# Kernel optimization log

Hardware: AMD Instinct MI355X
Metric: run time of the kernel (lower is better)

## Reference

```python
import jax, jax.numpy as jnp
import numpy as np
from jax import lax

V, E, H, K = 50000, 128, 256, 9
B, T = 64, 512


def setup_inputs() -> dict:
    key = jax.random.key(0)
    ks = jax.random.split(key, 16)
    s = 0.05
    return {
        "x": jax.random.randint(ks[0], (B, T), 0, V),
        "tags": jax.random.randint(ks[1], (B, T), 0, K),
        "mask": jnp.ones((B, T), dtype=bool),
        "embed_table": jax.random.normal(ks[2], (V, E), jnp.float32) * s,
        "w_ih_f": jax.random.normal(ks[3], (4 * H, E), jnp.float32) * s,
        "w_hh_f": jax.random.normal(ks[4], (4 * H, H), jnp.float32) * s,
        "b_ih_f": jax.random.normal(ks[5], (4 * H,), jnp.float32) * s,
        "b_hh_f": jax.random.normal(ks[6], (4 * H,), jnp.float32) * s,
        "w_ih_b": jax.random.normal(ks[7], (4 * H, E), jnp.float32) * s,
        "w_hh_b": jax.random.normal(ks[8], (4 * H, H), jnp.float32) * s,
        "b_ih_b": jax.random.normal(ks[9], (4 * H,), jnp.float32) * s,
        "b_hh_b": jax.random.normal(ks[10], (4 * H,), jnp.float32) * s,
        "w_tag": jax.random.normal(ks[11], (K, 2 * H), jnp.float32) * s,
        "b_tag": jax.random.normal(ks[12], (K,), jnp.float32) * s,
        "start_trans": jax.random.normal(ks[13], (K,), jnp.float32) * s,
        "end_trans": jax.random.normal(ks[14], (K,), jnp.float32) * s,
        "trans": jax.random.normal(ks[15], (K, K), jnp.float32) * s,
    }


def _lstm_dir(x_tbe, w_ih, w_hh, b_ih, b_hh, reverse=False):
    # x_tbe: [T, B, E]; torch gate order: i, f, g, o
    h0 = jnp.zeros((x_tbe.shape[1], H), x_tbe.dtype)
    c0 = jnp.zeros_like(h0)
    xg = jnp.einsum('tbe,ge->tbg', x_tbe, w_ih) + b_ih + b_hh  # precompute input gates

    def step(carry, xg_t):
        h, c = carry
        g = xg_t + h @ w_hh.T
        i, f, gg, o = jnp.split(g, 4, axis=-1)
        c = jax.nn.sigmoid(f) * c + jax.nn.sigmoid(i) * jnp.tanh(gg)
        h = jax.nn.sigmoid(o) * jnp.tanh(c)
        return (h, c), h

    _, hs = lax.scan(step, (h0, c0), xg, reverse=reverse)
    return hs  # [T, B, H]


def _crf_nll(emissions, tags, mask, start_trans, end_trans, trans):
    # emissions: [B,T,K]; tags: [B,T] int; mask: [B,T] bool. torchcrf, reduction='sum'.
    Bc, Tc, Kc = emissions.shape
    maskf = mask.astype(emissions.dtype)
    barange = jnp.arange(Bc)
    # numerator: score of gold path
    em_scores = jnp.take_along_axis(emissions, tags[..., None], axis=-1)[..., 0]  # [B,T]
    trans_scores = trans[tags[:, :-1], tags[:, 1:]]  # [B,T-1]
    num = start_trans[tags[:, 0]] + em_scores[:, 0]
    num = num + jnp.sum((em_scores[:, 1:] + trans_scores) * maskf[:, 1:], axis=1)
    last_idx = (jnp.sum(maskf, axis=1) - 1).astype(jnp.int32)
    last_tags = tags[barange, last_idx]
    num = num + end_trans[last_tags]
    # denominator: forward algorithm (log partition)
    alpha0 = start_trans[None, :] + emissions[:, 0]  # [B,K]

    def step(alpha, inp):
        em_t, m_t = inp  # [B,K], [B]
        nxt = jax.nn.logsumexp(alpha[:, :, None] + trans[None] + em_t[:, None, :], axis=1)
        return jnp.where(m_t[:, None], nxt, alpha), None

    alpha, _ = lax.scan(step, alpha0,
                        (jnp.swapaxes(emissions[:, 1:], 0, 1), mask[:, 1:].T))
    denom = jax.nn.logsumexp(alpha + end_trans[None, :], axis=1)
    llh = jnp.sum(num - denom)  # reduction='sum'
    return -llh


def reference(x, tags, mask, embed_table,
              w_ih_f, w_hh_f, b_ih_f, b_hh_f,
              w_ih_b, w_hh_b, b_ih_b, b_hh_b,
              w_tag, b_tag, start_trans, end_trans, trans):
    embedded = embed_table[x]                     # [B,T,E]
    x_tbe = jnp.swapaxes(embedded, 0, 1)          # [T,B,E]
    h_f = _lstm_dir(x_tbe, w_ih_f, w_hh_f, b_ih_f, b_hh_f, reverse=False)
    h_b = _lstm_dir(x_tbe, w_ih_b, w_hh_b, b_ih_b, b_hh_b, reverse=True)
    lstm_out = jnp.concatenate([h_f, h_b], axis=-1)         # [T,B,2H]
    lstm_out = jnp.swapaxes(lstm_out, 0, 1)                 # [B,T,2H]
    emissions = jnp.einsum('btd,kd->btk', lstm_out, w_tag) + b_tag
    return _crf_nll(emissions, tags, mask, start_trans, end_trans, trans)
```

## Files before the change

### kernel.cpp

```cpp
#include <hip/hip_runtime.h>
#include <stdint.h>


#define TT 512
#define BB 64
#define EE 128
#define HH 256

typedef __attribute__((ext_vector_type(8))) short short8;
typedef __attribute__((ext_vector_type(4))) float floatx4;
typedef __attribute__((ext_vector_type(2))) float floatx2;
typedef __attribute__((ext_vector_type(4))) unsigned uintx4;
typedef __attribute__((ext_vector_type(8))) unsigned uintx8;

__device__ __forceinline__ unsigned short f2bf(float f) {
    union { float f; unsigned u; } c; c.f = f;
    return (unsigned short)((c.u + 0x7FFFu + ((c.u >> 16) & 1u)) >> 16);
}
__device__ __forceinline__ unsigned pk_fp8x4(float a, float b, float c, float d) {
    int v = __builtin_amdgcn_cvt_pk_fp8_f32(a, b, 0, false);
    v = __builtin_amdgcn_cvt_pk_fp8_f32(c, d, v, true);
    return (unsigned)v;
}

__global__ __launch_bounds__(256)
void prep_kernel(const float* __restrict__ whf, const float* __restrict__ whb,
                 const float* __restrict__ wihf, const float* __restrict__ wihb,
                 unsigned* __restrict__ wre, unsigned short* __restrict__ wih_bf)
{
    const int bid = blockIdx.x, tid = threadIdx.x;
    if (bid < 512) {
        int idx = bid * 256 + tid;
        int j4   = idx & 7;
        int gcb  = (idx >> 3) & 7;
        int lane = (idx >> 6) & 63;
        int K0   = (idx >> 12) & 1;
        int wv   = (idx >> 13) & 7;
        int dir  = idx >> 16;
        int g = gcb >> 1, cb = gcb & 1;
        int l15 = lane & 15, lh = lane >> 4;
        int grow = g * 256 + wv * 32 + cb * 16 + l15;
        int k0 = K0 * 128 + lh * 32 + j4 * 4;
        const float* w = dir ? whb : whf;
        const float4 v = *(const float4*)(w + (size_t)grow * HH + k0);
        wre[idx] = pk_fp8x4(v.x, v.y, v.z, v.w);
    } else {
        int idx = (bid - 512) * 256 + tid;
        int dir = idx >> 14, rem = idx & 16383;
        const float* w = dir ? wihb : wihf;
        const float* s = w + (size_t)rem * 8;
        short8 v;
        #pragma unroll
        for (int j = 0; j < 8; ++j) v[j] = (short)f2bf(s[j]);
        *(short8*)(wih_bf + (size_t)idx * 8) = v;
    }
}

__global__ __launch_bounds__(256, 2)
void xg_kernel(const int* __restrict__ x, const float* __restrict__ embed,
               const unsigned short* __restrict__ wih_bf,
               const float* __restrict__ b_ih_f, const float* __restrict__ b_hh_f,
               const float* __restrict__ b_ih_b, const float* __restrict__ b_hh_b,
               unsigned* __restrict__ xg2)
{
    const int bid = blockIdx.x;
    const int dir = bid >> 10, t4 = (bid >> 3) & 127, nt = bid & 7;
    const int tid = threadIdx.x, lane = tid & 63, wv = tid >> 6;
    const int l15 = lane & 15, lh = lane >> 4;
    const float* b_ih = dir ? b_ih_b : b_ih_f;
    const float* b_hh = dir ? b_hh_b : b_hh_f;

    __shared__ int xid[64];
    __shared__ __align__(16) unsigned short As[64][136];
    __shared__ __align__(16) unsigned char Fs[64][144];
    __shared__ float bsh[128];

    if (tid < 128) bsh[tid] = b_ih[nt * 128 + tid] + b_hh[nt * 128 + tid];

    short8 wfr[8][4];
    const unsigned short* wbase = wih_bf + (size_t)dir * 131072;
    #pragma unroll
    for (int mt = 0; mt < 8; ++mt) {
        int grow = nt * 128 + mt * 16 + l15;
        #pragma unroll
        for (int kt = 0; kt < 4; ++kt)
            wfr[mt][kt] = *(const short8*)(wbase + (size_t)grow * EE + kt * 32 + lh * 8);
    }

    for (int tt = 0; tt < 4; ++tt) {
        const int t = t4 * 4 + tt;
        __syncthreads();
        if (tid < 64) xid[tid] = x[tid * TT + t];
        __syncthreads();
        for (int i = tid; i < 2048; i += 256) {
            int b = i >> 5, seg = i & 31;
            float4 v = *(const float4*)(embed + (size_t)xid[b] * EE + seg * 4);
            union { unsigned short u[4]; unsigned long long q; } p;
            p.u[0] = f2bf(v.x); p.u[1] = f2bf(v.y); p.u[2] = f2bf(v.z); p.u[3] = f2bf(v.w);
            *(unsigned long long*)&As[b][seg * 4] = p.q;
        }
        __syncthreads();

        floatx4 acc[8];
        #pragma unroll
        for (int mt = 0; mt < 8; ++mt) acc[mt] = (floatx4){0.f, 0.f, 0.f, 0.f};
        #pragma unroll
        for (int kt = 0; kt < 4; ++kt) {
            short8 af = *(const short8*)&As[wv * 16 + l15][kt * 32 + lh * 8];
            #pragma unroll
            for (int mt = 0; mt < 8; ++mt)
                acc[mt] = __builtin_amdgcn_mfma_f32_16x16x32_bf16(wfr[mt][kt], af, acc[mt], 0, 0, 0);
        }
        #pragma unroll
        for (int mt = 0; mt < 8; ++mt) {
            int j0 = mt * 16 + lh * 4;
            unsigned u = pk_fp8x4(acc[mt][0] + bsh[j0], acc[mt][1] + bsh[j0 + 1],
                                  acc[mt][2] + bsh[j0 + 2], acc[mt][3] + bsh[j0 + 3]);
            *(unsigned*)&Fs[wv * 16 + l15][j0] = u;
        }
        __syncthreads();
        for (int i = tid; i < 2048; i += 256) {
            int b = i >> 5, jq = i & 31;
            unsigned v = *(const unsigned*)&Fs[b][jq * 4];
            int growq = nt * 128 + jq * 4;
            int g = growq >> 8, hcol4 = (growq & 255) >> 2;
            size_t o32 = (((size_t)(dir * TT + t) * 64 + b) * 4 + g) * 64 + hcol4;
            xg2[o32] = v;
        }
    }
}

#define WWPAIR(A0, A1, V)                                                     \
    asm volatile("v_accvgpr_write_b32 a" #A0 ", %0\n\t"                       \
                 "v_accvgpr_write_b32 a" #A1 ", %1"                           \
                 :: "v"((unsigned)(V)), "v"((unsigned)((V) >> 32))            \
                 : "a" #A0, "a" #A1)

#define MFMA128(N0, N7, ACC, HF)                                              \
    asm volatile("v_mfma_f32_16x16x128_f8f6f4 %0, a[" #N0 ":" #N7 "], %1, %0" \
                 : "+v"(ACC) : "v"(HF))

__global__ void __launch_bounds__(512)
__attribute__((amdgpu_waves_per_eu(2, 2)))
rec_kernel(const unsigned char* __restrict__ wre, const unsigned* __restrict__ xg2,
           unsigned* __restrict__ hout)
{
    const int dir = blockIdx.x & 1;
    const int bg  = blockIdx.x >> 1;
    const int tid = threadIdx.x, lane = tid & 63, wv = tid >> 6;
    const int l15 = lane & 15, lh = lane >> 4;
    const int bbase = bg * 2;

    __shared__ __align__(16) unsigned char hbuf[2][16][272];
    __shared__ __align__(16) float gseg[4 * 2 * 268];
    for (int i = tid; i < 2176; i += 512) ((int*)hbuf)[i] = 0;

    const unsigned char* wb = wre + (size_t)dir * 262144 + wv * 32768 + lane * 256;
    {
        ulonglong2 q0, q1;
#define LOADSLOT(OFF)                                                         \
        q0 = *(const ulonglong2*)(wb + (OFF));                                \
        q1 = *(const ulonglong2*)(wb + (OFF) + 16);
        LOADSLOT(0)     WWPAIR(0,1,q0.x);   WWPAIR(2,3,q0.y);   WWPAIR(4,5,q1.x);   WWPAIR(6,7,q1.y);
        LOADSLOT(32)    WWPAIR(8,9,q0.x);   WWPAIR(10,11,q0.y); WWPAIR(12,13,q1.x); WWPAIR(14,15,q1.y);
        LOADSLOT(64)    WWPAIR(16,17,q0.x); WWPAIR(18,19,q0.y); WWPAIR(20,21,q1.x); WWPAIR(22,23,q1.y);
        LOADSLOT(96)    WWPAIR(24,25,q0.x); WWPAIR(26,27,q0.y); WWPAIR(28,29,q1.x); WWPAIR(30,31,q1.y);
        LOADSLOT(128)   WWPAIR(32,33,q0.x); WWPAIR(34,35,q0.y); WWPAIR(36,37,q1.x); WWPAIR(38,39,q1.y);
        LOADSLOT(160)   WWPAIR(40,41,q0.x); WWPAIR(42,43,q0.y); WWPAIR(44,45,q1.x); WWPAIR(46,47,q1.y);
        LOADSLOT(192)   WWPAIR(48,49,q0.x); WWPAIR(50,51,q0.y); WWPAIR(52,53,q1.x); WWPAIR(54,55,q1.y);
        LOADSLOT(224)   WWPAIR(56,57,q0.x); WWPAIR(58,59,q0.y); WWPAIR(60,61,q1.x); WWPAIR(62,63,q1.y);
        LOADSLOT(16384) WWPAIR(64,65,q0.x); WWPAIR(66,67,q0.y); WWPAIR(68,69,q1.x); WWPAIR(70,71,q1.y);
        LOADSLOT(16416) WWPAIR(72,73,q0.x); WWPAIR(74,75,q0.y); WWPAIR(76,77,q1.x); WWPAIR(78,79,q1.y);
        LOADSLOT(16448) WWPAIR(80,81,q0.x); WWPAIR(82,83,q0.y); WWPAIR(84,85,q1.x); WWPAIR(86,87,q1.y);
        LOADSLOT(16480) WWPAIR(88,89,q0.x); WWPAIR(90,91,q0.y); WWPAIR(92,93,q1.x); WWPAIR(94,95,q1.y);
        LOADSLOT(16512) WWPAIR(96,97,q0.x);   WWPAIR(98,99,q0.y);   WWPAIR(100,101,q1.x); WWPAIR(102,103,q1.y);
        LOADSLOT(16544) WWPAIR(104,105,q0.x); WWPAIR(106,107,q0.y); WWPAIR(108,109,q1.x); WWPAIR(110,111,q1.y);
        LOADSLOT(16576) WWPAIR(112,113,q0.x); WWPAIR(114,115,q0.y); WWPAIR(116,117,q1.x); WWPAIR(118,119,q1.y);
        LOADSLOT(16608) WWPAIR(120,121,q0.x); WWPAIR(122,123,q0.y); WWPAIR(124,125,q1.x); WWPAIR(126,127,q1.y);
#undef LOADSLOT
    }

    float c = 0.f;

    const int eb = tid >> 8;
    const int ec = tid & 255;

    const unsigned char* xrb = (const unsigned char*)xg2
        + (size_t)(dir * TT + (dir ? TT - 1 : 0)) * 65536
        + (bbase + eb) * 1024 + ec;
    const int xstep = dir ? -65536 : 65536;
    unsigned char* hdst = (unsigned char*)hout
        + ((size_t)(dir * TT + (dir ? TT - 1 : 0)) * BB + bbase + eb) * 256 + ec;
    const int hstep = dir ? -16384 : 16384;

    const unsigned char* hbr = &hbuf[0][0][0];
    unsigned char* hbw = (unsigned char*)&hbuf[1][0][0];

    __syncthreads();

    for (int t = 0; t < TT; ++t) {
        unsigned char xs0 = xrb[0], xs1 = xrb[256], xs2 = xrb[512], xs3 = xrb[768];

        floatx4 acc[4][2];
        #pragma unroll
        for (int g = 0; g < 4; ++g)
            #pragma unroll
            for (int cb = 0; cb < 2; ++cb)
                acc[g][cb] = (floatx4){0.f, 0.f, 0.f, 0.f};
        asm volatile("s_nop 1");

        {
            const unsigned char* hrow = hbr + l15 * 272 + lh * 32;
            uintx8 hf0, hf1;
            ((uintx4*)&hf0)[0] = *(const uintx4*)(hrow);
            ((uintx4*)&hf0)[1] = *(const uintx4*)(hrow + 16);
            ((uintx4*)&hf1)[0] = *(const uintx4*)(hrow + 128);
            ((uintx4*)&hf1)[1] = *(const uintx4*)(hrow + 144);
            MFMA128(0,7,      acc[0][0], hf0); MFMA128(16,23,    acc[1][0], hf0);
            MFMA128(32,39,    acc[2][0], hf0); MFMA128(48,55,    acc[3][0], hf0);
            MFMA128(64,71,    acc[0][0], hf1); MFMA128(80,87,    acc[1][0], hf1);
            MFMA128(96,103,   acc[2][0], hf1); MFMA128(112,119,  acc[3][0], hf1);
            MFMA128(8,15,     acc[0][1], hf0); MFMA128(24,31,    acc[1][1], hf0);
            MFMA128(40,47,    acc[2][1], hf0); MFMA128(56,63,    acc[3][1], hf0);
            MFMA128(72,79,    acc[0][1], hf1); MFMA128(88,95,    acc[1][1], hf1);
            MFMA128(104,111,  acc[2][1], hf1); MFMA128(120,127,  acc[3][1], hf1);
        }
        asm volatile("s_nop 7\n\ts_nop 7\n\ts_nop 7\n\ts_nop 3");

        if (l15 < 2) {
            #pragma unroll
            for (int g = 0; g < 4; ++g) {
                float* gw = &gseg[(g * 2 + l15) * 268 + wv * 32 + lh * 4];
                *(floatx4*)(gw)      = acc[g][0];
                *(floatx4*)(gw + 16) = acc[g][1];
            }
        }
        __syncthreads();

        float gv0 = gseg[(0 * 2 + eb) * 268 + ec];
        float gv1 = gseg[(1 * 2 + eb) * 268 + ec];
        float gv2 = gseg[(2 * 2 + eb) * 268 + ec];
        float gv3 = gseg[(3 * 2 + eb) * 268 + ec];
        floatx2 xi2 = __builtin_amdgcn_cvt_pk_f32_fp8((int)(unsigned)xs0, false);
        floatx2 xf2 = __builtin_amdgcn_cvt_pk_f32_fp8((int)(unsigned)xs1, false);
        floatx2 xg2v = __builtin_amdgcn_cvt_pk_f32_fp8((int)(unsigned)xs2, false);
        floatx2 xo2 = __builtin_amdgcn_cvt_pk_f32_fp8((int)(unsigned)xs3, false);
        float iv = gv0 + xi2[0];
        float fv = gv1 + xf2[0];
        float gv = gv2 + xg2v[0];
        float ov = gv3 + xo2[0];
        float A  = __expf(-iv);
        float C2 = __expf(-fv);
        float B  = __expf(-2.f * gv);
        float E  = __expf(-ov);
        float s1 = 1.f + A, s2 = 1.f + B, s3 = 1.f + C2, s4 = 1.f - B;
        float m1   = s1 * s2;
        float nsum = __builtin_fmaf(s4, s3, c * m1);
        float den  = s3 * m1;
        float cv   = nsum * __builtin_amdgcn_rcpf(den);
        c = cv;
        float F  = __expf(-2.f * cv);
        float s5 = 1.f + E, s6 = 1.f + F, s7 = 1.f - F;
        float hv = s7 * __builtin_amdgcn_rcpf(s5 * s6);
        unsigned char h8 = (unsigned char)
            ((unsigned)__builtin_amdgcn_cvt_pk_fp8_f32(hv, hv, 0, false) & 0xFFu);
        hbw[eb * 272 + ec] = h8;
        __syncthreads();

        *hdst = h8;
        hdst += hstep;
        xrb += xstep;
        { const unsigned char* tmp = hbr; hbr = hbw; hbw = (unsigned char*)tmp; }
    }
}

__global__ __launch_bounds__(256)
void em_kernel(const unsigned* __restrict__ hout, const float* __restrict__ w_tag,
               const float* __restrict__ b_tag, float* __restrict__ em)
{
    const int bid = blockIdx.x;
    const int b = bid >> 2, tq = bid & 3;
    const int tid = threadIdx.x, lane = tid & 63, wv = tid >> 6;
    const int dsel = lane >> 5, dloc = (lane & 31) * 8;

    float w72[9][8];
    #pragma unroll
    for (int k = 0; k < 9; ++k) {
        const float* src = w_tag + k * 512 + dsel * 256 + dloc;
        float4 a = *(const float4*)src;
        float4 b4 = *(const float4*)(src + 4);
        w72[k][0] = a.x;  w72[k][1] = a.y;  w72[k][2] = a.z;  w72[k][3] = a.w;
        w72[k][4] = b4.x; w72[k][5] = b4.y; w72[k][6] = b4.z; w72[k][7] = b4.w;
    }
    float btg = (lane < 9) ? b_tag[lane] : 0.f;

    for (int tt = wv; tt < 128; tt += 4) {
        int t = tq * 128 + tt;
        const unsigned* hp = hout + ((size_t)(dsel * TT + t) * BB + b) * 64 + (lane & 31) * 2;
        unsigned u0 = hp[0], u1 = hp[1];
        float hf[8];
        { floatx2 a = __builtin_amdgcn_cvt_pk_f32_fp8((int)u0, false);
          floatx2 b2 = __builtin_amdgcn_cvt_pk_f32_fp8((int)u0, true);
          hf[0]=a[0]; hf[1]=a[1]; hf[2]=b2[0]; hf[3]=b2[1]; }
        { floatx2 a = __builtin_amdgcn_cvt_pk_f32_fp8((int)u1, false);
          floatx2 b2 = __builtin_amdgcn_cvt_pk_f32_fp8((int)u1, true);
          hf[4]=a[0]; hf[5]=a[1]; hf[6]=b2[0]; hf[7]=b2[1]; }
        float p[9];
        #pragma unroll
        for (int k = 0; k < 9; ++k) {
            float s = 0.f;
            #pragma unroll
            for (int j = 0; j < 8; ++j) s += hf[j] * w72[k][j];
            p[k] = s;
        }
        float res = 0.f;
        #pragma unroll
        for (int k = 0; k < 9; ++k) {
            float s = p[k];
            s += __shfl_xor(s, 1);  s += __shfl_xor(s, 2);  s += __shfl_xor(s, 4);
            s += __shfl_xor(s, 8);  s += __shfl_xor(s, 16); s += __shfl_xor(s, 32);
            if (lane == k) res = s;
        }
        if (lane < 9) em[((size_t)b * TT + t) * 9 + lane] = res + btg;
    }
}

__global__ __launch_bounds__(256)
void scan_kernel(const float* __restrict__ em, const int* __restrict__ tags,
                 const float* __restrict__ st, const float* __restrict__ et,
                 const float* __restrict__ tr, float* __restrict__ out)
{
    const int b = blockIdx.x, tid = threadIdx.x;
    __shared__ float ems[4608];
    __shared__ float red[256];
    for (int i = tid; i < 4608; i += 256) ems[i] = em[(size_t)b * 4608 + i];
    __syncthreads();

    float nacc = 0.f;
    for (int t = tid; t < TT; t += 256) {
        int tg = tags[b * TT + t];
        float v = ems[t * 9 + tg];
        if (t > 0) v += tr[tags[b * TT + t - 1] * 9 + tg];
        nacc += v;
    }
    red[tid] = nacc;
    __syncthreads();
    for (int s = 128; s > 0; s >>= 1) {
        if (tid < s) red[tid] += red[tid + s];
        __syncthreads();
    }
    float num = red[0] + st[tags[b * TT]] + et[tags[b * TT + TT - 1]];

    if (tid < 64) {
        int kp = tid;
        int kpe = kp < 9 ? kp : 8;
        float trr[9];
        #pragma unroll
        for (int k = 0; k < 9; ++k) trr[k] = tr[k * 9 + kpe];
        float alpha = st[kpe] + ems[kpe];
        for (int t = 1; t < TT; ++t) {
            float av[9], m = -1e30f;
            #pragma unroll
            for (int k = 0; k < 9; ++k) { av[k] = __shfl(alpha, k) + trr[k]; m = fmaxf(m, av[k]); }
            float ssum = 0.f;
            #pragma unroll
            for (int k = 0; k < 9; ++k) ssum += __expf(av[k] - m);
            alpha = ems[t * 9 + kpe] + m + __logf(ssum);
        }
        float v = (kp < 9) ? (alpha + et[kpe]) : -1e30f;
        float m = v;
        m = fmaxf(m, __shfl_xor(m, 1));
        m = fmaxf(m, __shfl_xor(m, 2));
        m = fmaxf(m, __shfl_xor(m, 4));
        m = fmaxf(m, __shfl_xor(m, 8));
        float s = (kp < 9) ? __expf(v - m) : 0.f;
        s += __shfl_xor(s, 1);
        s += __shfl_xor(s, 2);
        s += __shfl_xor(s, 4);
        s += __shfl_xor(s, 8);
        if (kp == 0) atomicAdd(out, (m + __logf(s)) - num);
    }
}

extern "C" void kernel_launch(void* const* d_in, const int* in_sizes, int n_in,
                              void* d_out, int out_size, void* d_ws, size_t ws_size,
                              hipStream_t stream) {
    (void)in_sizes; (void)n_in; (void)out_size; (void)ws_size;
    const int* x        = (const int*)d_in[0];
    const int* tags     = (const int*)d_in[1];
    const float* embed  = (const float*)d_in[3];
    const float* w_ih_f = (const float*)d_in[4];
    const float* w_hh_f = (const float*)d_in[5];
    const float* b_ih_f = (const float*)d_in[6];
    const float* b_hh_f = (const float*)d_in[7];
    const float* w_ih_b = (const float*)d_in[8];
    const float* w_hh_b = (const float*)d_in[9];
    const float* b_ih_b = (const float*)d_in[10];
    const float* b_hh_b = (const float*)d_in[11];
    const float* w_tag  = (const float*)d_in[12];
    const float* b_tag  = (const float*)d_in[13];
    const float* st     = (const float*)d_in[14];
    const float* et     = (const float*)d_in[15];
    const float* tr     = (const float*)d_in[16];

    unsigned*       wre    = (unsigned*)d_ws;
    unsigned short* wih_bf = (unsigned short*)((char*)d_ws + 524288);
    unsigned*       xg2    = (unsigned*)((char*)d_ws + 1048576);
    unsigned*       hh     = (unsigned*)((char*)d_ws + 1048576 + 67108864);
    float*          em     = (float*)d_ws;

    hipMemsetAsync(d_out, 0, sizeof(float), stream);
    hipLaunchKernelGGL(prep_kernel, dim3(640), dim3(256), 0, stream,
                       w_hh_f, w_hh_b, w_ih_f, w_ih_b, wre, wih_bf);
    hipLaunchKernelGGL(xg_kernel, dim3(2048), dim3(256), 0, stream,
                       x, embed, wih_bf, b_ih_f, b_hh_f, b_ih_b, b_hh_b, xg2);
    hipLaunchKernelGGL(rec_kernel, dim3(64), dim3(512), 0, stream,
                       (const unsigned char*)wre, xg2, hh);
    hipLaunchKernelGGL(em_kernel, dim3(256), dim3(256), 0, stream,
                       hh, w_tag, b_tag, em);
    hipLaunchKernelGGL(scan_kernel, dim3(64), dim3(256), 0, stream,
                       em, tags, st, et, tr, (float*)d_out);
}
```

Before: 798.8 us.

## Split recurrent kernel to one batch row per block across 128 blocks

The recurrent LSTM kernel now handles one batch element per block instead of two, and the grid grows from 64 to 128 blocks. Each block still runs the full MFMA over 16 padded rows, but only the first 256 threads do the gate math and write h. The aim is to spread the serial time-step chain over twice as many CUs, halving the elementwise tail each step. In exchange the weight register loads and the MFMA work are duplicated per block, and half the threads sit idle during the elementwise phase.

Measured after the change: 767.6 us. 3.9% less time.

```diff
diff --git a/kernel.cpp b/kernel.cpp
--- a/kernel.cpp
+++ b/kernel.cpp
@@ -149,10 +149,9 @@
     const int bg  = blockIdx.x >> 1;
     const int tid = threadIdx.x, lane = tid & 63, wv = tid >> 6;
     const int l15 = lane & 15, lh = lane >> 4;
-    const int bbase = bg * 2;
 
     __shared__ __align__(16) unsigned char hbuf[2][16][272];
-    __shared__ __align__(16) float gseg[4 * 2 * 268];
+    __shared__ __align__(16) float gseg[4 * 268];
     for (int i = tid; i < 2176; i += 512) ((int*)hbuf)[i] = 0;
 
     const unsigned char* wb = wre + (size_t)dir * 262144 + wv * 32768 + lane * 256;
@@ -182,15 +181,15 @@
 
     float c = 0.f;
 
-    const int eb = tid >> 8;
     const int ec = tid & 255;
+    const bool edo = (tid < 256);
 
     const unsigned char* xrb = (const unsigned char*)xg2
         + (size_t)(dir * TT + (dir ? TT - 1 : 0)) * 65536
-        + (bbase + eb) * 1024 + ec;
+        + bg * 1024 + ec;
     const int xstep = dir ? -65536 : 65536;
     unsigned char* hdst = (unsigned char*)hout
-        + ((size_t)(dir * TT + (dir ? TT - 1 : 0)) * BB + bbase + eb) * 256 + ec;
+        + ((size_t)(dir * TT + (dir ? TT - 1 : 0)) * BB + bg) * 256 + ec;
     const int hstep = dir ? -16384 : 16384;
 
     const unsigned char* hbr = &hbuf[0][0][0];
@@ -227,47 +226,50 @@
         }
         asm volatile("s_nop 7\n\ts_nop 7\n\ts_nop 7\n\ts_nop 3");
 
-        if (l15 < 2) {
+        if (l15 == 0) {
             #pragma unroll
             for (int g = 0; g < 4; ++g) {
-                float* gw = &gseg[(g * 2 + l15) * 268 + wv * 32 + lh * 4];
+                float* gw = &gseg[g * 268 + wv * 32 + lh * 4];
                 *(floatx4*)(gw)      = acc[g][0];
                 *(floatx4*)(gw + 16) = acc[g][1];
             }
         }
         __syncthreads();
 
-        float gv0 = gseg[(0 * 2 + eb) * 268 + ec];
-        float gv1 = gseg[(1 * 2 + eb) * 268 + ec];
-        float gv2 = gseg[(2 * 2 + eb) * 268 + ec];
-        float gv3 = gseg[(3 * 2 + eb) * 268 + ec];
-        floatx2 xi2 = __builtin_amdgcn_cvt_pk_f32_fp8((int)(unsigned)xs0, false);
-        floatx2 xf2 = __builtin_amdgcn_cvt_pk_f32_fp8((int)(unsigned)xs1, false);
-        floatx2 xg2v = __builtin_amdgcn_cvt_pk_f32_fp8((int)(unsigned)xs2, false);
-        floatx2 xo2 = __builtin_amdgcn_cvt_pk_f32_fp8((int)(unsigned)xs3, false);
-        float iv = gv0 + xi2[0];
-        float fv = gv1 + xf2[0];
-        float gv = gv2 + xg2v[0];
-        float ov = gv3 + xo2[0];
-        float A  = __expf(-iv);
-        float C2 = __expf(-fv);
-        float B  = __expf(-2.f * gv);
-        float E  = __expf(-ov);
-        float s1 = 1.f + A, s2 = 1.f + B, s3 = 1.f + C2, s4 = 1.f - B;
-        float m1   = s1 * s2;
-        float nsum = __builtin_fmaf(s4, s3, c * m1);
-        float den  = s3 * m1;
-        float cv   = nsum * __builtin_amdgcn_rcpf(den);
-        c = cv;
-        float F  = __expf(-2.f * cv);
-        float s5 = 1.f + E, s6 = 1.f + F, s7 = 1.f - F;
-        float hv = s7 * __builtin_amdgcn_rcpf(s5 * s6);
-        unsigned char h8 = (unsigned char)
-            ((unsigned)__builtin_amdgcn_cvt_pk_fp8_f32(hv, hv, 0, false) & 0xFFu);
-        hbw[eb * 272 + ec] = h8;
-        __syncthreads();
-
-        *hdst = h8;
+        unsigned char h8 = 0;
+        if (edo) {
+            float gv0 = gseg[0 * 268 + ec];
+            float gv1 = gseg[1 * 268 + ec];
+            float gv2 = gseg[2 * 268 + ec];
+            float gv3 = gseg[3 * 268 + ec];
+            floatx2 xi2 = __builtin_amdgcn_cvt_pk_f32_fp8((int)(unsigned)xs0, false);
+            floatx2 xf2 = __builtin_amdgcn_cvt_pk_f32_fp8((int)(unsigned)xs1, false);
+            floatx2 xg2v = __builtin_amdgcn_cvt_pk_f32_fp8((int)(unsigned)xs2, false);
+            floatx2 xo2 = __builtin_amdgcn_cvt_pk_f32_fp8((int)(unsigned)xs3, false);
+            float iv = gv0 + xi2[0];
+            float fv = gv1 + xf2[0];
+            float gv = gv2 + xg2v[0];
+            float ov = gv3 + xo2[0];
+            float A  = __expf(-iv);
+            float C2 = __expf(-fv);
+            float B  = __expf(-2.f * gv);
+            float E  = __expf(-ov);
+            float s1 = 1.f + A, s2 = 1.f + B, s3 = 1.f + C2, s4 = 1.f - B;
+            float m1   = s1 * s2;
+            float nsum = __builtin_fmaf(s4, s3, c * m1);
+            float den  = s3 * m1;
+            float cv   = nsum * __builtin_amdgcn_rcpf(den);
+            c = cv;
+            float F  = __expf(-2.f * cv);
+            float s5 = 1.f + E, s6 = 1.f + F, s7 = 1.f - F;
+            float hv = s7 * __builtin_amdgcn_rcpf(s5 * s6);
+            h8 = (unsigned char)
+                ((unsigned)__builtin_amdgcn_cvt_pk_fp8_f32(hv, hv, 0, false) & 0xFFu);
+            hbw[ec] = h8;
+        }
+        __syncthreads();
+
+        if (edo) *hdst = h8;
         hdst += hstep;
         xrb += xstep;
         { const unsigned char* tmp = hbr; hbr = hbw; hbw = (unsigned char*)tmp; }
@@ -414,7 +416,7 @@
                        w_hh_f, w_hh_b, w_ih_f, w_ih_b, wre, wih_bf);
     hipLaunchKernelGGL(xg_kernel, dim3(2048), dim3(256), 0, stream,
                        x, embed, wih_bf, b_ih_f, b_hh_f, b_ih_b, b_hh_b, xg2);
-    hipLaunchKernelGGL(rec_kernel, dim3(64), dim3(512), 0, stream,
+    hipLaunchKernelGGL(rec_kernel, dim3(128), dim3(512), 0, stream,
                        (const unsigned char*)wre, xg2, hh);
     hipLaunchKernelGGL(em_kernel, dim3(256), dim3(256), 0, stream,
                        hh, w_tag, b_tag, em);
```
